# Kernel optimization log

Hardware: AMD Instinct MI355X
Metric: run time of the kernel (lower is better)

Reference implementation:

```python
import jax, jax.numpy as jnp
import numpy as np

B = 16      # number of point clouds
N = 4096    # points per cloud (max after densify)
D = 3       # xyz


def setup_inputs() -> dict:
    key = jax.random.key(0)
    k1, k2 = jax.random.split(key)
    pred = jax.random.normal(k1, (B * N, D), dtype=jnp.float32)
    target = jax.random.normal(k2, (B * N, D), dtype=jnp.float32)
    # sorted segment ids, equal-sized clouds (faithful to to_dense_batch usage)
    batch = jnp.repeat(jnp.arange(B, dtype=jnp.int64), N)
    return {"pred": pred, "target": target, "batch": batch}


def to_dense_batch(x, batch, num_batches, max_n):
    # PyG to_dense_batch: scatter flat points into [B, max_n, D], zero-padded.
    ones = jnp.ones_like(batch)
    counts = jax.ops.segment_sum(ones, batch, num_segments=num_batches)
    offsets = jnp.concatenate([jnp.zeros((1,), batch.dtype), jnp.cumsum(counts)[:-1]])
    pos = jnp.arange(batch.shape[0], dtype=batch.dtype) - offsets[batch]
    dense = jnp.zeros((num_batches, max_n, x.shape[-1]), x.dtype)
    return dense.at[batch, pos].set(x)


def chamfer_distance(x, y):
    # squared-euclidean pairwise distances via the GEMM identity
    x2 = jnp.sum(x * x, axis=-1)                      # [B, N]
    y2 = jnp.sum(y * y, axis=-1)                      # [B, M]
    xy = jnp.einsum('bnd,bmd->bnm', x, y)             # [B, N, M]
    d = x2[:, :, None] + y2[:, None, :] - 2.0 * xy    # [B, N, M]
    cham_x = jnp.mean(jnp.min(d, axis=2), axis=1)     # mean over N of min over M
    cham_y = jnp.mean(jnp.min(d, axis=1), axis=1)     # mean over M of min over N
    # point_reduction='mean', batch_reduction='mean' (pytorch3d defaults)
    return jnp.mean(cham_x + cham_y)


def reference(pred, target, batch):
    x = to_dense_batch(pred, batch, B, N)
    y = to_dense_batch(target, batch, B, N)
    return chamfer_distance(x, y)
```

## Files before the change

### kernel.cpp

```cpp
#include <hip/hip_runtime.h>


namespace {

constexpr int kB = 16;
constexpr int kN = 4096;
constexpr int kPlane = kB * kN;
constexpr int kJS = 4;
constexpr int kJSL = kN / kJS;
constexpr float kScale = 1.0f / (float)(kB * kN);

typedef short bf16x8 __attribute__((ext_vector_type(8)));
typedef float f32x16 __attribute__((ext_vector_type(16)));
typedef unsigned short u16;

__device__ inline u16 bf16_rn(float f) {
  union { float f; unsigned u; } v; v.f = f;
  unsigned r = v.u + 0x7fffu + ((v.u >> 16) & 1u);
  return (u16)(r >> 16);
}
__device__ inline float bf16_f(u16 h) {
  union { unsigned u; float f; } v; v.u = (unsigned)h << 16;
  return v.f;
}
__device__ inline unsigned pk2(u16 lo, u16 hi) {
  return (unsigned)lo | ((unsigned)hi << 16);
}

__device__ inline float min3f(float a, float b, float c) {
  float d;
  asm("v_min3_f32 %0, %1, %2, %3" : "=v"(d) : "v"(a), "v"(b), "v"(c));
  return d;
}

__global__ void init_out(float* out) { out[0] = 0.0f; }

__global__ __launch_bounds__(256) void cd_prep(
    const float* __restrict__ pred, const float* __restrict__ targ,
    u16* __restrict__ Ab, u16* __restrict__ Bb, float* __restrict__ out) {
  const int p = blockIdx.x * 256 + threadIdx.x;
  if (p == 0) out[0] = 0.0f;
  const u16 one = 0x3F80;
  {
    const float a = pred[3 * p], c = pred[3 * p + 1], d = pred[3 * p + 2];
    const u16 ah = bf16_rn(a), ch = bf16_rn(c), dh = bf16_rn(d);
    const u16 al = bf16_rn(a - bf16_f(ah));
    const u16 cl = bf16_rn(c - bf16_f(ch));
    const u16 dl = bf16_rn(d - bf16_f(dh));
    const float s2 = fmaf(a, a, fmaf(c, c, d * d));
    const u16 s2h = bf16_rn(s2);
    const u16 s2l = bf16_rn(s2 - bf16_f(s2h));
    uint4 w0, w1;
    w0.x = pk2(ah, ch); w0.y = pk2(dh, al); w0.z = pk2(cl, dl); w0.w = pk2(ah, ch);
    w1.x = pk2(dh, s2h); w1.y = pk2(s2l, one); w1.z = pk2(one, al); w1.w = pk2(cl, dl);
    uint4* dst = reinterpret_cast<uint4*>(Ab + (size_t)p * 16);
    dst[0] = w0; dst[1] = w1;
  }
  {
    const float a = targ[3 * p], c = targ[3 * p + 1], d = targ[3 * p + 2];
    const u16 ah0 = bf16_rn(a), ch0 = bf16_rn(c), dh0 = bf16_rn(d);
    const u16 ah = bf16_rn(-2.0f * bf16_f(ah0));
    const u16 ch = bf16_rn(-2.0f * bf16_f(ch0));
    const u16 dh = bf16_rn(-2.0f * bf16_f(dh0));
    const u16 al = bf16_rn(-2.0f * bf16_f(bf16_rn(a - bf16_f(ah0))));
    const u16 cl = bf16_rn(-2.0f * bf16_f(bf16_rn(c - bf16_f(ch0))));
    const u16 dl = bf16_rn(-2.0f * bf16_f(bf16_rn(d - bf16_f(dh0))));
    const float s2 = fmaf(a, a, fmaf(c, c, d * d));
    const u16 s2h = bf16_rn(s2);
    const u16 s2l = bf16_rn(s2 - bf16_f(s2h));
    uint4 w0, w1;
    w0.x = pk2(ah, ch); w0.y = pk2(dh, ah); w0.z = pk2(ch, dh); w0.w = pk2(al, cl);
    w1.x = pk2(dl, one); w1.y = pk2(one, s2h); w1.z = pk2(s2l, al); w1.w = pk2(cl, dl);
    uint4* dst = reinterpret_cast<uint4*>(Bb + (size_t)p * 16);
    dst[0] = w0; dst[1] = w1;
  }
}

__global__ __launch_bounds__(256) void cd_mfma(
    const u16* __restrict__ Ab, const u16* __restrict__ Bb,
    float* __restrict__ colpart, float* __restrict__ rowpart) {
  __shared__ float clds[4 * kJSL];

  const int t = threadIdx.x;
  const int w = t >> 6, lane = t & 63;
  const int half = lane >> 5, l31 = lane & 31;
  const int chunk = blockIdx.x;
  const int cloud = blockIdx.y;
  const int slice = blockIdx.z;

  const int arow = cloud * kN + chunk * 128 + w * 32 + l31;
  const bf16x8 afrag = *(const bf16x8*)(Ab + (size_t)arow * 16 + half * 8);

  f32x16 zacc;
#pragma unroll
  for (int r = 0; r < 16; ++r) zacc[r] = 0.0f;
  float rmin[16];
#pragma unroll
  for (int r = 0; r < 16; ++r) rmin[r] = 1e30f;

  const u16* bbase = Bb + ((size_t)cloud * kN + slice * kJSL) * 16;
  constexpr int NT = kJSL / 64;
  const int jcol = l31 * 16 + half * 8;
  bf16x8 b0 = *(const bf16x8*)(bbase + jcol);
  bf16x8 b1 = *(const bf16x8*)(bbase + 32 * 16 + jcol);
  for (int jt = 0; jt < NT; ++jt) {
    const int nx = ((jt + 1) & (NT - 1)) * 64 * 16;
    const bf16x8 n0 = *(const bf16x8*)(bbase + nx + jcol);
    const bf16x8 n1 = *(const bf16x8*)(bbase + nx + 32 * 16 + jcol);
    const f32x16 s0 = __builtin_amdgcn_mfma_f32_32x32x16_bf16(afrag, b0, zacc, 0, 0, 0);
    const f32x16 s1 = __builtin_amdgcn_mfma_f32_32x32x16_bf16(afrag, b1, zacc, 0, 0, 0);
    float a0 = min3f(s0[0], s0[1], s0[2]);
    float a1 = min3f(s0[3], s0[4], s0[5]);
    float a2 = min3f(s0[6], s0[7], s0[8]);
    float a3 = min3f(s0[9], s0[10], s0[11]);
    float a4 = min3f(s0[12], s0[13], s0[14]);
    float cm0 = fminf(min3f(a0, a1, a2), min3f(a3, a4, s0[15]));
    float b0t = min3f(s1[0], s1[1], s1[2]);
    float b1t = min3f(s1[3], s1[4], s1[5]);
    float b2t = min3f(s1[6], s1[7], s1[8]);
    float b3t = min3f(s1[9], s1[10], s1[11]);
    float b4t = min3f(s1[12], s1[13], s1[14]);
    float cm1 = fminf(min3f(b0t, b1t, b2t), min3f(b3t, b4t, s1[15]));
#pragma unroll
    for (int r = 0; r < 16; ++r)
      asm("v_min3_f32 %0, %0, %1, %2" : "+v"(rmin[r]) : "v"(s0[r]), "v"(s1[r]));
    cm0 = fminf(cm0, __shfl_xor(cm0, 32, 64));
    cm1 = fminf(cm1, __shfl_xor(cm1, 32, 64));
    if (half == 0) {
      clds[w * kJSL + jt * 64 + l31] = cm0;
      clds[w * kJSL + jt * 64 + 32 + l31] = cm1;
    }
    b0 = n0; b1 = n1;
  }

#pragma unroll
  for (int st = 1; st < 32; st <<= 1) {
#pragma unroll
    for (int r = 0; r < 16; ++r)
      rmin[r] = fminf(rmin[r], __shfl_xor(rmin[r], st, 64));
  }
  if (l31 == 0) {
    float* rp = rowpart + ((size_t)slice * kB + cloud) * kN + chunk * 128 + w * 32;
#pragma unroll
    for (int r = 0; r < 16; ++r) {
      const int row = (r & 3) + 8 * (r >> 2) + 4 * half;
      rp[row] = rmin[r];
    }
  }

  __syncthreads();
  for (int j = t; j < kJSL; j += 256) {
    const float m = fminf(fminf(clds[j], clds[kJSL + j]),
                          fminf(clds[2 * kJSL + j], clds[3 * kJSL + j]));
    colpart[((size_t)cloud * 32 + chunk) * kN + slice * kJSL + j] = m;
  }
}

__global__ __launch_bounds__(256) void cd_reduce(
    const float* __restrict__ colpart, const float* __restrict__ rowpart,
    float* __restrict__ out) {
  const int u = blockIdx.x * 256 + threadIdx.x;
  const int cloud = u >> 12, p = u & (kN - 1);
  float rm = 1e30f;
#pragma unroll
  for (int s2 = 0; s2 < kJS; ++s2)
    rm = fminf(rm, rowpart[((size_t)s2 * kB + cloud) * kN + p]);
  const float* cp = colpart + (size_t)cloud * 32 * kN + p;
  float cm = 1e30f;
#pragma unroll 8
  for (int c = 0; c < 32; ++c) cm = fminf(cm, cp[(size_t)c * kN]);
  float s = rm + cm;
  for (int o = 32; o > 0; o >>= 1) s += __shfl_down(s, o, 64);
  __shared__ float wsum[4];
  const int lane = threadIdx.x & 63, wv = threadIdx.x >> 6;
  if (lane == 0) wsum[wv] = s;
  __syncthreads();
  if (threadIdx.x == 0)
    atomicAdd(out, (wsum[0] + wsum[1] + wsum[2] + wsum[3]) * kScale);
}

template <int KX>
__global__ __launch_bounds__(256) void chamfer_direct(
    const float* __restrict__ pred, const float* __restrict__ targ,
    float* __restrict__ out) {
  __shared__ float4 tA[128], tB[128];
  const int t = threadIdx.x;
  const int xb = blockIdx.x, b = blockIdx.y, dir = blockIdx.z;
  const float* __restrict__ X = dir ? targ : pred;
  const float* __restrict__ Y = dir ? pred : targ;
  float2 xx2[KX], xy2[KX], xz2[KX];
  float x2[KX], mn[KX];
  const int ibase = b * kN + xb * (256 * KX) + t;
#pragma unroll
  for (int k = 0; k < KX; ++k) {
    const int i = ibase + k * 256;
    const float a = X[3 * i], c = X[3 * i + 1], d = X[3 * i + 2];
    x2[k] = fmaf(a, a, fmaf(c, c, d * d));
    xx2[k] = make_float2(-2.0f * a, -2.0f * a);
    xy2[k] = make_float2(-2.0f * c, -2.0f * c);
    xz2[k] = make_float2(-2.0f * d, -2.0f * d);
    mn[k] = 1e30f;
  }
  for (int t0 = 0; t0 < kN; t0 += 256) {
    __syncthreads();
    if (t < 128) {
      const int j0 = 3 * (b * kN + t0 + 2 * t);
      const float a0 = Y[j0], c0 = Y[j0 + 1], d0 = Y[j0 + 2];
      const float a1 = Y[j0 + 3], c1 = Y[j0 + 4], d1 = Y[j0 + 5];
      tA[t] = make_float4(a0, a1, c0, c1);
      tB[t] = make_float4(d0, d1, fmaf(a0, a0, fmaf(c0, c0, d0 * d0)),
                          fmaf(a1, a1, fmaf(c1, c1, d1 * d1)));
    }
    __syncthreads();
    for (int jj = 0; jj < 128; ++jj) {
      const float4 qa = tA[jj], qb = tB[jj];
      const float2 qx = make_float2(qa.x, qa.y), qy = make_float2(qa.z, qa.w);
      const float2 qz = make_float2(qb.x, qb.y), qw = make_float2(qb.z, qb.w);
#pragma unroll
      for (int k = 0; k < KX; ++k) {
        float2 acc;
        asm("v_pk_fma_f32 %0, %1, %2, %3\n\t"
            "v_pk_fma_f32 %0, %4, %5, %0\n\t"
            "v_pk_fma_f32 %0, %6, %7, %0"
            : "=&v"(acc)
            : "v"(xz2[k]), "v"(qz), "v"(qw), "v"(xy2[k]), "v"(qy),
              "v"(xx2[k]), "v"(qx));
        asm("v_min3_f32 %0, %0, %1, %2" : "+v"(mn[k]) : "v"(acc.x), "v"(acc.y));
      }
    }
  }
  float s = 0.0f;
#pragma unroll
  for (int k = 0; k < KX; ++k) s += x2[k] + mn[k];
  for (int o = 32; o > 0; o >>= 1) s += __shfl_down(s, o, 64);
  __shared__ float wsum[4];
  const int lane = t & 63, wv = t >> 6;
  if (lane == 0) wsum[wv] = s;
  __syncthreads();
  if (t == 0)
    atomicAdd(out, (wsum[0] + wsum[1] + wsum[2] + wsum[3]) * kScale);
}

}

extern "C" void kernel_launch(void* const* d_in, const int* in_sizes, int n_in,
                              void* d_out, int out_size, void* d_ws,
                              size_t ws_size, hipStream_t stream) {
  const float* pred = (const float*)d_in[0];
  const float* targ = (const float*)d_in[1];
  float* out = (float*)d_out;

  const size_t needA = (size_t)kPlane * 16 * sizeof(u16);
  const size_t needCol = (size_t)kB * 32 * kN * sizeof(float);
  const size_t needRow = (size_t)kJS * kPlane * sizeof(float);
  if (ws_size >= 2 * needA + needCol + needRow) {
    u16* Ab = (u16*)d_ws;
    u16* Bb = (u16*)((char*)d_ws + needA);
    float* colpart = (float*)((char*)d_ws + 2 * needA);
    float* rowpart = (float*)((char*)d_ws + 2 * needA + needCol);
    cd_prep<<<dim3(kPlane / 256), 256, 0, stream>>>(pred, targ, Ab, Bb, out);
    cd_mfma<<<dim3(32, kB, kJS), 256, 0, stream>>>(Ab, Bb, colpart, rowpart);
    cd_reduce<<<dim3(kPlane / 256), 256, 0, stream>>>(colpart, rowpart, out);
  } else {
    init_out<<<dim3(1), dim3(1), 0, stream>>>(out);
    constexpr int KX = 8;
    dim3 grid(kN / (256 * KX), kB, 2);
    chamfer_direct<KX><<<grid, 256, 0, stream>>>(pred, targ, out);
  }
}
```

Before: 98.51 us.

## Fuse bf16 split-precision prep into MFMA kernel with swizzled LDS B tiles

Removes the separate prep kernel. Each MFMA block now builds its A fragment from pred in registers and builds the B operand for its target slice into XOR-swizzled shared memory, instead of reading both from a global workspace. The number of j-slices doubles (kJS 4->8), which halves the per-block LDS footprint and adds more blocks and more row partials. This saves one launch and a global round trip, but each target slice's conversion is now recomputed by every chunk block, and the extra slices add work for cd_reduce.

```diff
diff --git a/kernel.cpp b/kernel.cpp
--- a/kernel.cpp
+++ b/kernel.cpp
@@ -6,7 +6,7 @@
 constexpr int kB = 16;
 constexpr int kN = 4096;
 constexpr int kPlane = kB * kN;
-constexpr int kJS = 4;
+constexpr int kJS = 8;
 constexpr int kJSL = kN / kJS;
 constexpr float kScale = 1.0f / (float)(kB * kN);
 
@@ -35,14 +35,28 @@
 
 __global__ void init_out(float* out) { out[0] = 0.0f; }
 
-__global__ __launch_bounds__(256) void cd_prep(
+__global__ __launch_bounds__(256) void cd_mfma(
     const float* __restrict__ pred, const float* __restrict__ targ,
-    u16* __restrict__ Ab, u16* __restrict__ Bb, float* __restrict__ out) {
-  const int p = blockIdx.x * 256 + threadIdx.x;
-  if (p == 0) out[0] = 0.0f;
+    float* __restrict__ colpart, float* __restrict__ rowpart,
+    float* __restrict__ out) {
+  __shared__ uint4 Blds4[kJSL * 2];
+  __shared__ float clds[4 * kJSL];
+
+  const int t = threadIdx.x;
+  const int w = t >> 6, lane = t & 63;
+  const int half = lane >> 5, l31 = lane & 31;
+  const int chunk = blockIdx.x;
+  const int cloud = blockIdx.y;
+  const int slice = blockIdx.z;
+
+  if ((t | chunk | cloud | slice) == 0) out[0] = 0.0f;
+
   const u16 one = 0x3F80;
+
+  const int arow = cloud * kN + chunk * 128 + w * 32 + l31;
+  union { uint4 u; bf16x8 v; } afu;
   {
-    const float a = pred[3 * p], c = pred[3 * p + 1], d = pred[3 * p + 2];
+    const float a = pred[3 * arow], c = pred[3 * arow + 1], d = pred[3 * arow + 2];
     const u16 ah = bf16_rn(a), ch = bf16_rn(c), dh = bf16_rn(d);
     const u16 al = bf16_rn(a - bf16_f(ah));
     const u16 cl = bf16_rn(c - bf16_f(ch));
@@ -50,46 +64,40 @@
     const float s2 = fmaf(a, a, fmaf(c, c, d * d));
     const u16 s2h = bf16_rn(s2);
     const u16 s2l = bf16_rn(s2 - bf16_f(s2h));
-    uint4 w0, w1;
-    w0.x = pk2(ah, ch); w0.y = pk2(dh, al); w0.z = pk2(cl, dl); w0.w = pk2(ah, ch);
-    w1.x = pk2(dh, s2h); w1.y = pk2(s2l, one); w1.z = pk2(one, al); w1.w = pk2(cl, dl);
-    uint4* dst = reinterpret_cast<uint4*>(Ab + (size_t)p * 16);
-    dst[0] = w0; dst[1] = w1;
-  }
+    if (half == 0) {
+      afu.u.x = pk2(ah, ch); afu.u.y = pk2(dh, al);
+      afu.u.z = pk2(cl, dl); afu.u.w = pk2(ah, ch);
+    } else {
+      afu.u.x = pk2(dh, s2h); afu.u.y = pk2(s2l, one);
+      afu.u.z = pk2(one, al); afu.u.w = pk2(cl, dl);
+    }
+  }
+  const bf16x8 afrag = afu.v;
+
   {
-    const float a = targ[3 * p], c = targ[3 * p + 1], d = targ[3 * p + 2];
-    const u16 ah0 = bf16_rn(a), ch0 = bf16_rn(c), dh0 = bf16_rn(d);
-    const u16 ah = bf16_rn(-2.0f * bf16_f(ah0));
-    const u16 ch = bf16_rn(-2.0f * bf16_f(ch0));
-    const u16 dh = bf16_rn(-2.0f * bf16_f(dh0));
-    const u16 al = bf16_rn(-2.0f * bf16_f(bf16_rn(a - bf16_f(ah0))));
-    const u16 cl = bf16_rn(-2.0f * bf16_f(bf16_rn(c - bf16_f(ch0))));
-    const u16 dl = bf16_rn(-2.0f * bf16_f(bf16_rn(d - bf16_f(dh0))));
-    const float s2 = fmaf(a, a, fmaf(c, c, d * d));
-    const u16 s2h = bf16_rn(s2);
-    const u16 s2l = bf16_rn(s2 - bf16_f(s2h));
-    uint4 w0, w1;
-    w0.x = pk2(ah, ch); w0.y = pk2(dh, ah); w0.z = pk2(ch, dh); w0.w = pk2(al, cl);
-    w1.x = pk2(dl, one); w1.y = pk2(one, s2h); w1.z = pk2(s2l, al); w1.w = pk2(cl, dl);
-    uint4* dst = reinterpret_cast<uint4*>(Bb + (size_t)p * 16);
-    dst[0] = w0; dst[1] = w1;
-  }
-}
-
-__global__ __launch_bounds__(256) void cd_mfma(
-    const u16* __restrict__ Ab, const u16* __restrict__ Bb,
-    float* __restrict__ colpart, float* __restrict__ rowpart) {
-  __shared__ float clds[4 * kJSL];
-
-  const int t = threadIdx.x;
-  const int w = t >> 6, lane = t & 63;
-  const int half = lane >> 5, l31 = lane & 31;
-  const int chunk = blockIdx.x;
-  const int cloud = blockIdx.y;
-  const int slice = blockIdx.z;
-
-  const int arow = cloud * kN + chunk * 128 + w * 32 + l31;
-  const bf16x8 afrag = *(const bf16x8*)(Ab + (size_t)arow * 16 + half * 8);
+    const float* tb = targ + (size_t)(cloud * kN + slice * kJSL) * 3;
+    char* bl = (char*)Blds4;
+    for (int pl = t; pl < kJSL; pl += 256) {
+      const float a = tb[3 * pl], c = tb[3 * pl + 1], d = tb[3 * pl + 2];
+      const u16 ah0 = bf16_rn(a), ch0 = bf16_rn(c), dh0 = bf16_rn(d);
+      const u16 ah = bf16_rn(-2.0f * bf16_f(ah0));
+      const u16 ch = bf16_rn(-2.0f * bf16_f(ch0));
+      const u16 dh = bf16_rn(-2.0f * bf16_f(dh0));
+      const u16 al = bf16_rn(-2.0f * bf16_f(bf16_rn(a - bf16_f(ah0))));
+      const u16 cl = bf16_rn(-2.0f * bf16_f(bf16_rn(c - bf16_f(ch0))));
+      const u16 dl = bf16_rn(-2.0f * bf16_f(bf16_rn(d - bf16_f(dh0))));
+      const float s2 = fmaf(a, a, fmaf(c, c, d * d));
+      const u16 s2h = bf16_rn(s2);
+      const u16 s2l = bf16_rn(s2 - bf16_f(s2h));
+      uint4 w0, w1;
+      w0.x = pk2(ah, ch); w0.y = pk2(dh, ah); w0.z = pk2(ch, dh); w0.w = pk2(al, cl);
+      w1.x = pk2(dl, one); w1.y = pk2(one, s2h); w1.z = pk2(s2l, al); w1.w = pk2(cl, dl);
+      const int sw = (pl & 7) << 4;
+      *reinterpret_cast<uint4*>(bl + ((pl * 32) ^ sw)) = w0;
+      *reinterpret_cast<uint4*>(bl + ((pl * 32 + 16) ^ sw)) = w1;
+    }
+  }
+  __syncthreads();
 
   f32x16 zacc;
 #pragma unroll
@@ -98,17 +106,16 @@
 #pragma unroll
   for (int r = 0; r < 16; ++r) rmin[r] = 1e30f;
 
-  const u16* bbase = Bb + ((size_t)cloud * kN + slice * kJSL) * 16;
   constexpr int NT = kJSL / 64;
-  const int jcol = l31 * 16 + half * 8;
-  bf16x8 b0 = *(const bf16x8*)(bbase + jcol);
-  bf16x8 b1 = *(const bf16x8*)(bbase + 32 * 16 + jcol);
+  const char* bl = (const char*)Blds4;
+  int addr0 = (l31 * 32 + half * 16) ^ ((l31 & 7) << 4);
   for (int jt = 0; jt < NT; ++jt) {
-    const int nx = ((jt + 1) & (NT - 1)) * 64 * 16;
-    const bf16x8 n0 = *(const bf16x8*)(bbase + nx + jcol);
-    const bf16x8 n1 = *(const bf16x8*)(bbase + nx + 32 * 16 + jcol);
-    const f32x16 s0 = __builtin_amdgcn_mfma_f32_32x32x16_bf16(afrag, b0, zacc, 0, 0, 0);
-    const f32x16 s1 = __builtin_amdgcn_mfma_f32_32x32x16_bf16(afrag, b1, zacc, 0, 0, 0);
+    union { uint4 u; bf16x8 v; } B0, B1;
+    B0.u = *reinterpret_cast<const uint4*>(bl + addr0);
+    B1.u = *reinterpret_cast<const uint4*>(bl + addr0 + 1024);
+    addr0 += 2048;
+    const f32x16 s0 = __builtin_amdgcn_mfma_f32_32x32x16_bf16(afrag, B0.v, zacc, 0, 0, 0);
+    const f32x16 s1 = __builtin_amdgcn_mfma_f32_32x32x16_bf16(afrag, B1.v, zacc, 0, 0, 0);
     float a0 = min3f(s0[0], s0[1], s0[2]);
     float a1 = min3f(s0[3], s0[4], s0[5]);
     float a2 = min3f(s0[6], s0[7], s0[8]);
@@ -130,7 +137,6 @@
       clds[w * kJSL + jt * 64 + l31] = cm0;
       clds[w * kJSL + jt * 64 + 32 + l31] = cm1;
     }
-    b0 = n0; b1 = n1;
   }
 
 #pragma unroll
@@ -250,16 +256,13 @@
   const float* targ = (const float*)d_in[1];
   float* out = (float*)d_out;
 
-  const size_t needA = (size_t)kPlane * 16 * sizeof(u16);
   const size_t needCol = (size_t)kB * 32 * kN * sizeof(float);
   const size_t needRow = (size_t)kJS * kPlane * sizeof(float);
-  if (ws_size >= 2 * needA + needCol + needRow) {
-    u16* Ab = (u16*)d_ws;
-    u16* Bb = (u16*)((char*)d_ws + needA);
-    float* colpart = (float*)((char*)d_ws + 2 * needA);
-    float* rowpart = (float*)((char*)d_ws + 2 * needA + needCol);
-    cd_prep<<<dim3(kPlane / 256), 256, 0, stream>>>(pred, targ, Ab, Bb, out);
-    cd_mfma<<<dim3(32, kB, kJS), 256, 0, stream>>>(Ab, Bb, colpart, rowpart);
+  if (ws_size >= needCol + needRow) {
+    float* colpart = (float*)d_ws;
+    float* rowpart = (float*)((char*)d_ws + needCol);
+    cd_mfma<<<dim3(32, kB, kJS), 256, 0, stream>>>(pred, targ, colpart,
+                                                   rowpart, out);
     cd_reduce<<<dim3(kPlane / 256), 256, 0, stream>>>(colpart, rowpart, out);
   } else {
     init_out<<<dim3(1), dim3(1), 0, stream>>>(out);
```

After: 100.8 us. 1.02x slower.
